# Kernel tuning notes

Measured on AMD Instinct MI355X. Metric: run time of the kernel, lower is better.

## Reference

```python
import jax, jax.numpy as jnp
import numpy as np

BETA = 0.25
SCALE_NUM = 4  # len(latents_scale)


def setup_inputs() -> dict:
    key = jax.random.key(0)
    kz, ke = jax.random.split(key)
    z = jax.random.normal(kz, (8, 256, 32, 32), dtype=jnp.float32)
    emb_weight = jax.random.normal(ke, (16384, 256), dtype=jnp.float32) * 0.02
    return {"z": z, "emb_weight": emb_weight}


def reference(z, emb_weight):
    # z: [B, C, H, W] with C == vq_embed_dim and H == W (source reshapes with W twice)
    B, C, H, W = z.shape
    z_det = jax.lax.stop_gradient(z)

    # NOTE: in the source, `residual` is flattened ONCE before the scale loop and
    # never updated inside it, so every scale picks the same indices. We compute
    # the nearest-codebook assignment once (identical math, argmin of cdist is
    # invariant under sqrt, so squared distances suffice).
    residual = jnp.transpose(z_det, (0, 2, 3, 1)).reshape(-1, C)  # [N, D], N=B*H*W
    d2 = (jnp.sum(residual * residual, axis=1, keepdims=True)
          - 2.0 * residual @ emb_weight.T
          + jnp.sum(emb_weight * emb_weight, axis=1))  # [N, n_e]
    idx = jnp.argmin(d2, axis=1).reshape(B, W, W)  # [B, W, W]

    quantized = jnp.transpose(emb_weight[idx], (0, 3, 1, 2))  # [B, C, H, W]

    z_hat = jnp.zeros_like(z_det)
    loss = jnp.float32(0.0)
    for _ in range(SCALE_NUM):
        z_hat = z_hat + quantized
        loss = loss + BETA * jnp.mean((jax.lax.stop_gradient(z_hat) - z) ** 2) \
                    + jnp.mean((z_hat - z_det) ** 2)
    loss = loss / SCALE_NUM

    total_idx = jnp.concatenate([idx] * SCALE_NUM, axis=1)  # [B, SCALE_NUM*W, W]
    z_hat_out = z + jax.lax.stop_gradient(z_hat - z)  # straight-through
    return z_hat_out, loss, total_idx
```

## Files before the change

### kernel.cpp

```cpp
#include <hip/hip_runtime.h>

#define D      256
#define N_E    16384
#define NPTS   8192
#define ZOUT   2097152
#define MARGIN 2.0e-2f
#define STRIPS 4

typedef short bf16x8 __attribute__((ext_vector_type(8)));
typedef unsigned short us8 __attribute__((ext_vector_type(8)));
typedef float f32x16 __attribute__((ext_vector_type(16)));
typedef unsigned long long u64;

__device__ __forceinline__ unsigned short f2bf(float x) {
    unsigned int u = __float_as_uint(x);
    return (unsigned short)((u + 0x7FFFu + ((u >> 16) & 1u)) >> 16);
}
__device__ __forceinline__ void gl_lds16(const void* g, void* l) {
    __builtin_amdgcn_global_load_lds(
        (const __attribute__((address_space(1))) unsigned int*)g,
        (__attribute__((address_space(3))) unsigned int*)l, 16, 0, 0);
}

__global__ __launch_bounds__(256) void prep(
    const float* __restrict__ z, const float* __restrict__ emb,
    unsigned short* __restrict__ Zpk, float* __restrict__ Zf32,
    unsigned short* __restrict__ Epk, float* __restrict__ e2) {
    const int t = threadIdx.x;
    if (blockIdx.x < 256) {
        const int n0 = blockIdx.x * 32;
        const int p = t & 31, ks8 = t >> 5;
        const int n = n0 + p;
        const int b = n >> 10, hw = n & 1023;
        const float* zb = z + (size_t)b * 262144 + hw;
        const int k0 = ks8 * 32;
        float v[32];
        #pragma unroll
        for (int kk = 0; kk < 32; ++kk)
            v[kk] = zb[(size_t)(k0 + kk) * 1024];
        #pragma unroll
        for (int i = 0; i < 8; ++i) {
            float4 f = {v[i * 4], v[i * 4 + 1], v[i * 4 + 2], v[i * 4 + 3]};
            *(float4*)(Zf32 + (size_t)n * D + k0 + i * 4) = f;
        }
        const int g = n >> 5;
        #pragma unroll
        for (int i = 0; i < 4; ++i) {
            us8 hv;
            #pragma unroll
            for (int c = 0; c < 8; ++c) hv[c] = f2bf(-2.0f * v[i * 8 + c]);
            const int kabs = k0 + i * 8;
            const int ks = kabs >> 4;
            const int l = (n & 31) + ((kabs >> 3) & 1) * 32;
            *(us8*)(Zpk + ((size_t)(g * 16 + ks) * 64 + l) * 8) = hv;
        }
    } else {
        const int j0 = (blockIdx.x - 256) * 32;
        const int jj = j0 + (t >> 3), q = t & 7;
        const float* row = emb + (size_t)jj * D + q * 32;
        float v[32];
        float s = 0.f;
        #pragma unroll
        for (int i = 0; i < 8; ++i) {
            const float4 x = *(const float4*)(row + i * 4);
            v[i * 4] = x.x; v[i * 4 + 1] = x.y; v[i * 4 + 2] = x.z; v[i * 4 + 3] = x.w;
            s += x.x * x.x + x.y * x.y + x.z * x.z + x.w * x.w;
        }
        const int g = jj >> 5;
        #pragma unroll
        for (int i = 0; i < 4; ++i) {
            us8 hv;
            #pragma unroll
            for (int c = 0; c < 8; ++c) hv[c] = f2bf(v[i * 8 + c]);
            const int kabs = q * 32 + i * 8;
            const int ks = kabs >> 4;
            const int l = (jj & 31) + ((kabs >> 3) & 1) * 32;
            *(us8*)(Epk + ((size_t)(g * 16 + ks) * 64 + l) * 8) = hv;
        }
        s += __shfl_xor(s, 1);
        s += __shfl_xor(s, 2);
        s += __shfl_xor(s, 4);
        if (q == 0) e2[jj] = s;
    }
}

__global__ __launch_bounds__(256, 2) void mfma_gemm(
    const unsigned short* __restrict__ Epk, const unsigned short* __restrict__ Zpk,
    const float* __restrict__ e2, float* __restrict__ tminv,
    u64* __restrict__ tmask) {
    __shared__ unsigned short Zbuf[64 * 512];

    const int tid = threadIdx.x, lane = tid & 63, wid = tid >> 6;
    const int c32 = lane & 31, l5 = lane >> 5;
    const int n0 = blockIdx.x * 128;
    const int cs0 = blockIdx.y * (STRIPS * 256);

    #pragma unroll
    for (int ks = 0; ks < 16; ++ks)
        gl_lds16(Zpk + ((size_t)((n0 >> 5) + wid) * 16 + ks) * 512 + lane * 8,
                 Zbuf + (wid * 16 + ks) * 512);
    __syncthreads();

    for (int s = 0; s < STRIPS; ++s) {
        const int cb = cs0 + s * 256 + wid * 64;
        const unsigned short* eb = Epk + ((size_t)(cb >> 5) * 16) * 512 + lane * 8;
        const unsigned short* zb = Zbuf + lane * 8;

        f32x16 acc[2][4];
        const f32x16 z16 = {0.f};
        #pragma unroll
        for (int i = 0; i < 2; ++i)
            #pragma unroll
            for (int j = 0; j < 4; ++j) acc[i][j] = z16;

        bf16x8 ec[2], pc[4];
        ec[0] = *(const bf16x8*)(eb);
        ec[1] = *(const bf16x8*)(eb + 16 * 512);
        #pragma unroll
        for (int j = 0; j < 4; ++j) pc[j] = *(const bf16x8*)(zb + (j * 16) * 512);

        #pragma unroll 4
        for (int ks = 0; ks < 16; ++ks) {
            bf16x8 en[2], pn[4];
            if (ks < 15) {
                en[0] = *(const bf16x8*)(eb + (ks + 1) * 512);
                en[1] = *(const bf16x8*)(eb + (16 + ks + 1) * 512);
                #pragma unroll
                for (int j = 0; j < 4; ++j)
                    pn[j] = *(const bf16x8*)(zb + (j * 16 + ks + 1) * 512);
            }
            #pragma unroll
            for (int i = 0; i < 2; ++i)
                #pragma unroll
                for (int j = 0; j < 4; ++j)
                    acc[i][j] = __builtin_amdgcn_mfma_f32_32x32x16_bf16(
                        ec[i], pc[j], acc[i][j], 0, 0, 0);
            if (ks < 15) {
                ec[0] = en[0]; ec[1] = en[1];
                #pragma unroll
                for (int j = 0; j < 4; ++j) pc[j] = pn[j];
            }
        }

        float e2r[2][16];
        #pragma unroll
        for (int i = 0; i < 2; ++i)
            #pragma unroll
            for (int r = 0; r < 16; ++r)
                e2r[i][r] = e2[cb + i * 32 + (r & 3) + 8 * (r >> 2) + 4 * l5];
        #pragma unroll
        for (int j = 0; j < 4; ++j) {
            float m = e2r[0][0] + acc[0][j][0];
            #pragma unroll
            for (int r = 1; r < 16; ++r) m = fminf(m, e2r[0][r] + acc[0][j][r]);
            #pragma unroll
            for (int r = 0; r < 16; ++r) m = fminf(m, e2r[1][r] + acc[1][j][r]);
            m = fminf(m, __shfl_xor(m, 32));
            const float th = m + MARGIN;
            unsigned mk[2];
            #pragma unroll
            for (int i = 0; i < 2; ++i) {
                unsigned mm = 0;
                #pragma unroll
                for (int r = 0; r < 16; ++r) {
                    const int row = (r & 3) + 8 * (r >> 2) + 4 * l5;
                    mm |= (e2r[i][r] + acc[i][j][r] <= th) ? (1u << row) : 0u;
                }
                mk[i] = mm | (unsigned)__shfl_xor((int)mm, 32);
            }
            if (l5 == 0) {
                const size_t pt = (size_t)(n0 + j * 32 + c32);
                tminv[pt * 256 + (cb >> 6)] = m;
                tmask[pt * 256 + (cb >> 6)] = ((u64)mk[1] << 32) | (u64)mk[0];
            }
        }
    }
}

__global__ __launch_bounds__(256) void rescore(
    const float* __restrict__ tminv, const u64* __restrict__ tmask,
    const float* __restrict__ Zf32, const float* __restrict__ emb,
    const float* __restrict__ e2, int* __restrict__ idxf,
    float* __restrict__ out_idx, float* __restrict__ loss) {
    const int tid = threadIdx.x, lane = tid & 63, w = tid >> 6;
    const int n = blockIdx.x * 4 + w;
    if (blockIdx.x == 0 && tid == 0) loss[0] = 0.f;

    const float4 zr = *(const float4*)(Zf32 + (size_t)n * D + lane * 4);
    const float4 tv = *(const float4*)(tminv + (size_t)n * 256 + lane * 4);

    float m1 = fminf(fminf(tv.x, tv.y), fminf(tv.z, tv.w));
    #pragma unroll
    for (int st = 1; st < 64; st <<= 1) m1 = fminf(m1, __shfl_xor(m1, st));
    const float thresh = m1 + MARGIN;

    u64 best = ~0ull;
    const float tva[4] = {tv.x, tv.y, tv.z, tv.w};
    #pragma unroll
    for (int k = 0; k < 4; ++k) {
        u64 gm = __ballot(tva[k] <= thresh);
        while (gm) {
            const int bit = (int)__builtin_ctzll(gm);
            gm &= gm - 1;
            const int g = bit * 4 + k;
            u64 cm = tmask[(size_t)n * 256 + g];
            while (cm) {
                const int r = (int)__builtin_ctzll(cm);
                cm &= cm - 1;
                const int c = g * 64 + r;
                const float4 ev = *(const float4*)(emb + (size_t)c * D + lane * 4);
                float s = zr.x * ev.x + zr.y * ev.y + zr.z * ev.z + zr.w * ev.w;
                #pragma unroll
                for (int st = 1; st < 64; st <<= 1) s += __shfl_xor(s, st);
                const float d = e2[c] - 2.0f * s;
                unsigned int u = __float_as_uint(d);
                u = (u & 0x80000000u) ? ~u : (u | 0x80000000u);
                const u64 key = ((u64)u << 32) | (unsigned int)c;
                if (key < best) best = key;
            }
        }
    }
    if (lane == 0) {
        const int bi = (int)(unsigned int)(best & 0xFFFFFFFFull);
        idxf[n] = bi;
        const int b = n >> 10, hw = n & 1023;
        const float fv = (float)bi;
        #pragma unroll
        for (int sc = 0; sc < 4; ++sc) out_idx[b * 4096 + sc * 1024 + hw] = fv;
    }
}

__global__ __launch_bounds__(256) void quant_loss(
    const float* __restrict__ z, const float* __restrict__ emb,
    const int* __restrict__ idxf, float* __restrict__ out,
    float* __restrict__ loss) {
    __shared__ int idx_l[32];
    __shared__ float wsum[4];
    const int blk = blockIdx.x;
    const int c0 = (blk >> 8) * 64;
    const int rem = blk & 255;
    const int b = rem >> 5, hw0 = (rem & 31) * 32;
    const int t = threadIdx.x, hw_l = t & 31, cg = t >> 5;
    if (t < 32) idx_l[t] = idxf[b * 1024 + hw0 + t];
    __syncthreads();
    const int j = idx_l[hw_l];
    const float* er = emb + (size_t)j * D + c0 + cg * 8;
    const float4 q0 = *(const float4*)er;
    const float4 q1 = *(const float4*)(er + 4);
    const float qv[8] = {q0.x, q0.y, q0.z, q0.w, q1.x, q1.y, q1.z, q1.w};
    float e = 0.f;
    #pragma unroll
    for (int cc = 0; cc < 8; ++cc) {
        const int c = c0 + cg * 8 + cc;
        const size_t zi = (size_t)b * 262144 + (size_t)c * 1024 + hw0 + hw_l;
        const float zv = z[zi];
        const float q = qv[cc];
        const float zh = ((q + q) + q) + q;
        out[zi] = zv + (zh - zv);
        e += 30.0f * q * q - 20.0f * q * zv + 4.0f * zv * zv;
    }
    #pragma unroll
    for (int off = 32; off > 0; off >>= 1) e += __shfl_down(e, off);
    if ((t & 63) == 0) wsum[t >> 6] = e;
    __syncthreads();
    if (t == 0) {
        const float s = wsum[0] + wsum[1] + wsum[2] + wsum[3];
        atomicAdd(loss, s * (0.3125f / 2097152.0f));
    }
}

extern "C" void kernel_launch(void* const* d_in, const int* in_sizes, int n_in,
                              void* d_out, int out_size, void* d_ws, size_t ws_size,
                              hipStream_t stream) {
    const float* z = (const float*)d_in[0];
    const float* emb = (const float*)d_in[1];
    float* out = (float*)d_out;

    unsigned short* Zpk = (unsigned short*)d_ws;
    unsigned short* Epk = Zpk + (size_t)NPTS * D;
    float* Zf32 = (float*)(Epk + (size_t)N_E * D);
    float* e2 = Zf32 + (size_t)NPTS * D;
    float* tminv = e2 + N_E;
    u64* tmask = (u64*)(tminv + (size_t)NPTS * 256);
    int* idxf = (int*)(tmask + (size_t)NPTS * 256);

    float* loss = out + ZOUT;
    float* out_idx = out + ZOUT + 1;

    prep<<<768, 256, 0, stream>>>(z, emb, Zpk, Zf32, Epk, e2);
    mfma_gemm<<<dim3(NPTS / 128, N_E / (256 * STRIPS)), 256, 0, stream>>>(
        Epk, Zpk, e2, tminv, tmask);
    rescore<<<NPTS / 4, 256, 0, stream>>>(tminv, tmask, Zf32, emb, e2, idxf,
                                          out_idx, loss);
    quant_loss<<<1024, 256, 0, stream>>>(z, emb, idxf, out, loss);
}
```

Before: 176.1 us.

## Fold codebook norms into MFMA, coarsen candidate masks, 4-codeword rescoring

Codebook squared norms are packed as split hi/lo bf16 pairs and added into the accumulators through an extra MFMA against a ones vector, which removes the per-element e2 loads and adds in the epilogue. The candidate mask is coarsened to 16 bits per 64-codeword group, one bit per 4 rows, so tmask shrinks to u16. Rescoring now evaluates 4 codewords at once per wavefront, 16 lanes each, and reduces the keys across lanes. The operand loads in the GEMM loop are double-buffered two steps ahead. In exchange, the coarser masks pull in more false candidates for rescoring, and the bf16 split of e2 lowers the precision of the screening distances.

```diff
diff --git a/kernel.cpp b/kernel.cpp
--- a/kernel.cpp
+++ b/kernel.cpp
@@ -16,6 +16,9 @@
     unsigned int u = __float_as_uint(x);
     return (unsigned short)((u + 0x7FFFu + ((u >> 16) & 1u)) >> 16);
 }
+__device__ __forceinline__ float bf2f(unsigned short h) {
+    return __uint_as_float((unsigned int)h << 16);
+}
 __device__ __forceinline__ void gl_lds16(const void* g, void* l) {
     __builtin_amdgcn_global_load_lds(
         (const __attribute__((address_space(1))) unsigned int*)g,
@@ -25,7 +28,9 @@
 __global__ __launch_bounds__(256) void prep(
     const float* __restrict__ z, const float* __restrict__ emb,
     unsigned short* __restrict__ Zpk, float* __restrict__ Zf32,
-    unsigned short* __restrict__ Epk, float* __restrict__ e2) {
+    unsigned short* __restrict__ Epk, float* __restrict__ e2,
+    unsigned short* __restrict__ E2pk) {
+    __shared__ float sh[32];
     const int t = threadIdx.x;
     if (blockIdx.x < 256) {
         const int n0 = blockIdx.x * 32;
@@ -80,14 +85,27 @@
         s += __shfl_xor(s, 1);
         s += __shfl_xor(s, 2);
         s += __shfl_xor(s, 4);
-        if (q == 0) e2[jj] = s;
+        if (q == 0) { e2[jj] = s; sh[t >> 3] = s; }
+        __syncthreads();
+        if (t < 64) {
+            us8 hv;
+            #pragma unroll
+            for (int c = 0; c < 8; ++c) hv[c] = 0;
+            if (t < 32) {
+                const float vv = sh[t];
+                const unsigned short hi = f2bf(vv);
+                hv[0] = hi;
+                hv[1] = f2bf(vv - bf2f(hi));
+            }
+            *(us8*)(E2pk + (size_t)(blockIdx.x - 256) * 512 + t * 8) = hv;
+        }
     }
 }
 
 __global__ __launch_bounds__(256, 2) void mfma_gemm(
     const unsigned short* __restrict__ Epk, const unsigned short* __restrict__ Zpk,
-    const float* __restrict__ e2, float* __restrict__ tminv,
-    u64* __restrict__ tmask) {
+    const unsigned short* __restrict__ E2pk, float* __restrict__ tminv,
+    unsigned short* __restrict__ tmask) {
     __shared__ unsigned short Zbuf[64 * 512];
 
     const int tid = threadIdx.x, lane = tid & 63, wid = tid >> 6;
@@ -95,6 +113,12 @@
     const int n0 = blockIdx.x * 128;
     const int cs0 = blockIdx.y * (STRIPS * 256);
 
+    us8 puu;
+    #pragma unroll
+    for (int c = 0; c < 8; ++c) puu[c] = 0;
+    if (l5 == 0) { puu[0] = 0x3F80; puu[1] = 0x3F80; }
+    const bf16x8 pu = (bf16x8)puu;
+
     #pragma unroll
     for (int ks = 0; ks < 16; ++ks)
         gl_lds16(Zpk + ((size_t)((n0 >> 5) + wid) * 16 + ks) * 512 + lane * 8,
@@ -106,6 +130,9 @@
         const unsigned short* eb = Epk + ((size_t)(cb >> 5) * 16) * 512 + lane * 8;
         const unsigned short* zb = Zbuf + lane * 8;
 
+        const bf16x8 e2f0 = *(const bf16x8*)(E2pk + (size_t)(cb >> 5) * 512 + lane * 8);
+        const bf16x8 e2f1 = *(const bf16x8*)(E2pk + ((size_t)(cb >> 5) + 1) * 512 + lane * 8);
+
         f32x16 acc[2][4];
         const f32x16 z16 = {0.f};
         #pragma unroll
@@ -113,72 +140,80 @@
             #pragma unroll
             for (int j = 0; j < 4; ++j) acc[i][j] = z16;
 
-        bf16x8 ec[2], pc[4];
-        ec[0] = *(const bf16x8*)(eb);
-        ec[1] = *(const bf16x8*)(eb + 16 * 512);
-        #pragma unroll
-        for (int j = 0; j < 4; ++j) pc[j] = *(const bf16x8*)(zb + (j * 16) * 512);
+        bf16x8 eq[2][2], pq[2][4];
+        #pragma unroll
+        for (int par = 0; par < 2; ++par) {
+            eq[par][0] = *(const bf16x8*)(eb + par * 512);
+            eq[par][1] = *(const bf16x8*)(eb + (16 + par) * 512);
+            #pragma unroll
+            for (int j = 0; j < 4; ++j)
+                pq[par][j] = *(const bf16x8*)(zb + (j * 16 + par) * 512);
+        }
 
         #pragma unroll 4
         for (int ks = 0; ks < 16; ++ks) {
-            bf16x8 en[2], pn[4];
-            if (ks < 15) {
-                en[0] = *(const bf16x8*)(eb + (ks + 1) * 512);
-                en[1] = *(const bf16x8*)(eb + (16 + ks + 1) * 512);
+            const int p = ks & 1;
+            const bf16x8 ec0 = eq[p][0], ec1 = eq[p][1];
+            const bf16x8 pc0 = pq[p][0], pc1 = pq[p][1];
+            const bf16x8 pc2 = pq[p][2], pc3 = pq[p][3];
+            if (ks < 14) {
+                eq[p][0] = *(const bf16x8*)(eb + (ks + 2) * 512);
+                eq[p][1] = *(const bf16x8*)(eb + (16 + ks + 2) * 512);
                 #pragma unroll
                 for (int j = 0; j < 4; ++j)
-                    pn[j] = *(const bf16x8*)(zb + (j * 16 + ks + 1) * 512);
+                    pq[p][j] = *(const bf16x8*)(zb + (j * 16 + ks + 2) * 512);
             }
+            acc[0][0] = __builtin_amdgcn_mfma_f32_32x32x16_bf16(ec0, pc0, acc[0][0], 0, 0, 0);
+            acc[0][1] = __builtin_amdgcn_mfma_f32_32x32x16_bf16(ec0, pc1, acc[0][1], 0, 0, 0);
+            acc[0][2] = __builtin_amdgcn_mfma_f32_32x32x16_bf16(ec0, pc2, acc[0][2], 0, 0, 0);
+            acc[0][3] = __builtin_amdgcn_mfma_f32_32x32x16_bf16(ec0, pc3, acc[0][3], 0, 0, 0);
+            acc[1][0] = __builtin_amdgcn_mfma_f32_32x32x16_bf16(ec1, pc0, acc[1][0], 0, 0, 0);
+            acc[1][1] = __builtin_amdgcn_mfma_f32_32x32x16_bf16(ec1, pc1, acc[1][1], 0, 0, 0);
+            acc[1][2] = __builtin_amdgcn_mfma_f32_32x32x16_bf16(ec1, pc2, acc[1][2], 0, 0, 0);
+            acc[1][3] = __builtin_amdgcn_mfma_f32_32x32x16_bf16(ec1, pc3, acc[1][3], 0, 0, 0);
+        }
+        #pragma unroll
+        for (int j = 0; j < 4; ++j) {
+            acc[0][j] = __builtin_amdgcn_mfma_f32_32x32x16_bf16(e2f0, pu, acc[0][j], 0, 0, 0);
+            acc[1][j] = __builtin_amdgcn_mfma_f32_32x32x16_bf16(e2f1, pu, acc[1][j], 0, 0, 0);
+        }
+
+        #pragma unroll
+        for (int j = 0; j < 4; ++j) {
+            float cm[2][4];
             #pragma unroll
             for (int i = 0; i < 2; ++i)
                 #pragma unroll
-                for (int j = 0; j < 4; ++j)
-                    acc[i][j] = __builtin_amdgcn_mfma_f32_32x32x16_bf16(
-                        ec[i], pc[j], acc[i][j], 0, 0, 0);
-            if (ks < 15) {
-                ec[0] = en[0]; ec[1] = en[1];
-                #pragma unroll
-                for (int j = 0; j < 4; ++j) pc[j] = pn[j];
-            }
-        }
-
-        float e2r[2][16];
-        #pragma unroll
-        for (int i = 0; i < 2; ++i)
-            #pragma unroll
-            for (int r = 0; r < 16; ++r)
-                e2r[i][r] = e2[cb + i * 32 + (r & 3) + 8 * (r >> 2) + 4 * l5];
-        #pragma unroll
-        for (int j = 0; j < 4; ++j) {
-            float m = e2r[0][0] + acc[0][j][0];
-            #pragma unroll
-            for (int r = 1; r < 16; ++r) m = fminf(m, e2r[0][r] + acc[0][j][r]);
-            #pragma unroll
-            for (int r = 0; r < 16; ++r) m = fminf(m, e2r[1][r] + acc[1][j][r]);
+                for (int q = 0; q < 4; ++q) {
+                    float t0 = fminf(acc[i][j][q * 4], acc[i][j][q * 4 + 1]);
+                    t0 = fminf(t0, acc[i][j][q * 4 + 2]);
+                    cm[i][q] = fminf(t0, acc[i][j][q * 4 + 3]);
+                }
+            float m = fminf(cm[0][0], cm[0][1]);
+            m = fminf(m, cm[0][2]); m = fminf(m, cm[0][3]);
+            m = fminf(m, cm[1][0]); m = fminf(m, cm[1][1]);
+            m = fminf(m, cm[1][2]); m = fminf(m, cm[1][3]);
             m = fminf(m, __shfl_xor(m, 32));
             const float th = m + MARGIN;
-            unsigned mk[2];
-            #pragma unroll
-            for (int i = 0; i < 2; ++i) {
-                unsigned mm = 0;
+            unsigned mm = 0;
+            #pragma unroll
+            for (int i = 0; i < 2; ++i)
                 #pragma unroll
-                for (int r = 0; r < 16; ++r) {
-                    const int row = (r & 3) + 8 * (r >> 2) + 4 * l5;
-                    mm |= (e2r[i][r] + acc[i][j][r] <= th) ? (1u << row) : 0u;
-                }
-                mk[i] = mm | (unsigned)__shfl_xor((int)mm, 32);
-            }
+                for (int q = 0; q < 4; ++q)
+                    mm |= (cm[i][q] <= th) ? (1u << (i * 8 + 2 * q)) : 0u;
+            mm <<= l5;
+            mm |= (unsigned)__shfl_xor((int)mm, 32);
             if (l5 == 0) {
                 const size_t pt = (size_t)(n0 + j * 32 + c32);
                 tminv[pt * 256 + (cb >> 6)] = m;
-                tmask[pt * 256 + (cb >> 6)] = ((u64)mk[1] << 32) | (u64)mk[0];
+                tmask[pt * 256 + (cb >> 6)] = (unsigned short)mm;
             }
         }
     }
 }
 
 __global__ __launch_bounds__(256) void rescore(
-    const float* __restrict__ tminv, const u64* __restrict__ tmask,
+    const float* __restrict__ tminv, const unsigned short* __restrict__ tmask,
     const float* __restrict__ Zf32, const float* __restrict__ emb,
     const float* __restrict__ e2, int* __restrict__ idxf,
     float* __restrict__ out_idx, float* __restrict__ loss) {
@@ -186,9 +221,13 @@
     const int n = blockIdx.x * 4 + w;
     if (blockIdx.x == 0 && tid == 0) loss[0] = 0.f;
 
-    const float4 zr = *(const float4*)(Zf32 + (size_t)n * D + lane * 4);
+    const int sl = lane & 15, qr = lane >> 4;
+    float4 zs[4];
+    #pragma unroll
+    for (int p = 0; p < 4; ++p)
+        zs[p] = *(const float4*)(Zf32 + (size_t)n * D + p * 64 + sl * 4);
+
     const float4 tv = *(const float4*)(tminv + (size_t)n * 256 + lane * 4);
-
     float m1 = fminf(fminf(tv.x, tv.y), fminf(tv.z, tv.w));
     #pragma unroll
     for (int st = 1; st < 64; st <<= 1) m1 = fminf(m1, __shfl_xor(m1, st));
@@ -203,19 +242,30 @@
             const int bit = (int)__builtin_ctzll(gm);
             gm &= gm - 1;
             const int g = bit * 4 + k;
-            u64 cm = tmask[(size_t)n * 256 + g];
+            unsigned cm = tmask[(size_t)n * 256 + g];
             while (cm) {
-                const int r = (int)__builtin_ctzll(cm);
+                const int cl = (int)__builtin_ctz(cm);
                 cm &= cm - 1;
-                const int c = g * 64 + r;
-                const float4 ev = *(const float4*)(emb + (size_t)c * D + lane * 4);
-                float s = zr.x * ev.x + zr.y * ev.y + zr.z * ev.z + zr.w * ev.w;
+                const int c0 = g * 64 + cl * 4;
+                const int c = c0 + qr;
+                const float* er = emb + (size_t)c * D;
+                float sacc = 0.f;
                 #pragma unroll
-                for (int st = 1; st < 64; st <<= 1) s += __shfl_xor(s, st);
-                const float d = e2[c] - 2.0f * s;
+                for (int p = 0; p < 4; ++p) {
+                    const float4 ev = *(const float4*)(er + p * 64 + sl * 4);
+                    sacc += ev.x * zs[p].x + ev.y * zs[p].y +
+                            ev.z * zs[p].z + ev.w * zs[p].w;
+                }
+                sacc += __shfl_xor(sacc, 1);
+                sacc += __shfl_xor(sacc, 2);
+                sacc += __shfl_xor(sacc, 4);
+                sacc += __shfl_xor(sacc, 8);
+                const float d = e2[c] - 2.0f * sacc;
                 unsigned int u = __float_as_uint(d);
                 u = (u & 0x80000000u) ? ~u : (u | 0x80000000u);
-                const u64 key = ((u64)u << 32) | (unsigned int)c;
+                u64 key = ((u64)u << 32) | (unsigned int)c;
+                u64 o = __shfl_xor(key, 16); if (o < key) key = o;
+                o = __shfl_xor(key, 32); if (o < key) key = o;
                 if (key < best) best = key;
             }
         }
@@ -281,15 +331,16 @@
     float* Zf32 = (float*)(Epk + (size_t)N_E * D);
     float* e2 = Zf32 + (size_t)NPTS * D;
     float* tminv = e2 + N_E;
-    u64* tmask = (u64*)(tminv + (size_t)NPTS * 256);
-    int* idxf = (int*)(tmask + (size_t)NPTS * 256);
+    unsigned short* tmask = (unsigned short*)(tminv + (size_t)NPTS * 256);
+    unsigned short* E2pk = tmask + (size_t)NPTS * 256;
+    int* idxf = (int*)(E2pk + (size_t)512 * 512);
 
     float* loss = out + ZOUT;
     float* out_idx = out + ZOUT + 1;
 
-    prep<<<768, 256, 0, stream>>>(z, emb, Zpk, Zf32, Epk, e2);
+    prep<<<768, 256, 0, stream>>>(z, emb, Zpk, Zf32, Epk, e2, E2pk);
     mfma_gemm<<<dim3(NPTS / 128, N_E / (256 * STRIPS)), 256, 0, stream>>>(
-        Epk, Zpk, e2, tminv, tmask);
+        Epk, Zpk, E2pk, tminv, tmask);
     rescore<<<NPTS / 4, 256, 0, stream>>>(tminv, tmask, Zf32, emb, e2, idxf,
                                           out_idx, loss);
     quant_loss<<<1024, 256, 0, stream>>>(z, emb, idxf, out, loss);
```

Result: slower. 192.1 us (+9.1%).

## Fuse rescore and quantize-loss kernels into one per-32-point block kernel

Applied to the files above, without the earlier changes.

Merges the candidate rescoring kernel and the quantization/loss kernel into a single kernel with 1024-thread blocks covering 32 points. The selected indices stay in shared memory instead of going through a global index buffer, which removes one launch and one global round trip. Loss zeroing moves into the prep kernel. The grid shrinks to 256 large blocks, each wave handling two points serially, which may lower parallelism and occupancy for the irregular rescoring loop.

```diff
diff --git a/kernel.cpp b/kernel.cpp
--- a/kernel.cpp
+++ b/kernel.cpp
@@ -25,8 +25,10 @@
 __global__ __launch_bounds__(256) void prep(
     const float* __restrict__ z, const float* __restrict__ emb,
     unsigned short* __restrict__ Zpk, float* __restrict__ Zf32,
-    unsigned short* __restrict__ Epk, float* __restrict__ e2) {
+    unsigned short* __restrict__ Epk, float* __restrict__ e2,
+    float* __restrict__ loss) {
     const int t = threadIdx.x;
+    if (blockIdx.x == 0 && t == 0) loss[0] = 0.f;
     if (blockIdx.x < 256) {
         const int n0 = blockIdx.x * 32;
         const int p = t & 31, ks8 = t >> 5;
@@ -177,81 +179,77 @@
     }
 }
 
-__global__ __launch_bounds__(256) void rescore(
+__global__ __launch_bounds__(1024) void rescore_quant(
     const float* __restrict__ tminv, const u64* __restrict__ tmask,
     const float* __restrict__ Zf32, const float* __restrict__ emb,
-    const float* __restrict__ e2, int* __restrict__ idxf,
-    float* __restrict__ out_idx, float* __restrict__ loss) {
-    const int tid = threadIdx.x, lane = tid & 63, w = tid >> 6;
-    const int n = blockIdx.x * 4 + w;
-    if (blockIdx.x == 0 && tid == 0) loss[0] = 0.f;
-
-    const float4 zr = *(const float4*)(Zf32 + (size_t)n * D + lane * 4);
-    const float4 tv = *(const float4*)(tminv + (size_t)n * 256 + lane * 4);
-
-    float m1 = fminf(fminf(tv.x, tv.y), fminf(tv.z, tv.w));
-    #pragma unroll
-    for (int st = 1; st < 64; st <<= 1) m1 = fminf(m1, __shfl_xor(m1, st));
-    const float thresh = m1 + MARGIN;
-
-    u64 best = ~0ull;
-    const float tva[4] = {tv.x, tv.y, tv.z, tv.w};
-    #pragma unroll
-    for (int k = 0; k < 4; ++k) {
-        u64 gm = __ballot(tva[k] <= thresh);
-        while (gm) {
-            const int bit = (int)__builtin_ctzll(gm);
-            gm &= gm - 1;
-            const int g = bit * 4 + k;
-            u64 cm = tmask[(size_t)n * 256 + g];
-            while (cm) {
-                const int r = (int)__builtin_ctzll(cm);
-                cm &= cm - 1;
-                const int c = g * 64 + r;
-                const float4 ev = *(const float4*)(emb + (size_t)c * D + lane * 4);
-                float s = zr.x * ev.x + zr.y * ev.y + zr.z * ev.z + zr.w * ev.w;
-                #pragma unroll
-                for (int st = 1; st < 64; st <<= 1) s += __shfl_xor(s, st);
-                const float d = e2[c] - 2.0f * s;
-                unsigned int u = __float_as_uint(d);
-                u = (u & 0x80000000u) ? ~u : (u | 0x80000000u);
-                const u64 key = ((u64)u << 32) | (unsigned int)c;
-                if (key < best) best = key;
-            }
-        }
-    }
-    if (lane == 0) {
-        const int bi = (int)(unsigned int)(best & 0xFFFFFFFFull);
-        idxf[n] = bi;
-        const int b = n >> 10, hw = n & 1023;
-        const float fv = (float)bi;
-        #pragma unroll
-        for (int sc = 0; sc < 4; ++sc) out_idx[b * 4096 + sc * 1024 + hw] = fv;
-    }
-}
-
-__global__ __launch_bounds__(256) void quant_loss(
-    const float* __restrict__ z, const float* __restrict__ emb,
-    const int* __restrict__ idxf, float* __restrict__ out,
+    const float* __restrict__ e2, const float* __restrict__ z,
+    float* __restrict__ out, float* __restrict__ out_idx,
     float* __restrict__ loss) {
-    __shared__ int idx_l[32];
-    __shared__ float wsum[4];
-    const int blk = blockIdx.x;
-    const int c0 = (blk >> 8) * 64;
-    const int rem = blk & 255;
-    const int b = rem >> 5, hw0 = (rem & 31) * 32;
-    const int t = threadIdx.x, hw_l = t & 31, cg = t >> 5;
-    if (t < 32) idx_l[t] = idxf[b * 1024 + hw0 + t];
+    __shared__ int idx_s[32];
+    __shared__ float wsum[16];
+    const int tid = threadIdx.x, lane = tid & 63, wd = tid >> 6;
+    const int n0 = blockIdx.x * 32;
+    const int b = n0 >> 10, hw0 = n0 & 1023;
+
+    #pragma unroll 1
+    for (int p = 0; p < 2; ++p) {
+        const int lp = wd * 2 + p;
+        const int n = n0 + lp;
+        const float4 zr = *(const float4*)(Zf32 + (size_t)n * D + lane * 4);
+        const float4 tv = *(const float4*)(tminv + (size_t)n * 256 + lane * 4);
+
+        float m1 = fminf(fminf(tv.x, tv.y), fminf(tv.z, tv.w));
+        #pragma unroll
+        for (int st = 1; st < 64; st <<= 1) m1 = fminf(m1, __shfl_xor(m1, st));
+        const float thresh = m1 + MARGIN;
+
+        u64 best = ~0ull;
+        const float tva[4] = {tv.x, tv.y, tv.z, tv.w};
+        #pragma unroll
+        for (int k = 0; k < 4; ++k) {
+            u64 gm = __ballot(tva[k] <= thresh);
+            while (gm) {
+                const int bit = (int)__builtin_ctzll(gm);
+                gm &= gm - 1;
+                const int g = bit * 4 + k;
+                u64 cm = tmask[(size_t)n * 256 + g];
+                while (cm) {
+                    const int r = (int)__builtin_ctzll(cm);
+                    cm &= cm - 1;
+                    const int c = g * 64 + r;
+                    const float4 ev = *(const float4*)(emb + (size_t)c * D + lane * 4);
+                    float s = zr.x * ev.x + zr.y * ev.y + zr.z * ev.z + zr.w * ev.w;
+                    #pragma unroll
+                    for (int st = 1; st < 64; st <<= 1) s += __shfl_xor(s, st);
+                    const float d = e2[c] - 2.0f * s;
+                    unsigned int u = __float_as_uint(d);
+                    u = (u & 0x80000000u) ? ~u : (u | 0x80000000u);
+                    const u64 key = ((u64)u << 32) | (unsigned int)c;
+                    if (key < best) best = key;
+                }
+            }
+        }
+        if (lane == 0)
+            idx_s[lp] = (int)(unsigned int)(best & 0xFFFFFFFFull);
+    }
     __syncthreads();
-    const int j = idx_l[hw_l];
-    const float* er = emb + (size_t)j * D + c0 + cg * 8;
+
+    if (tid < 32) {
+        const float fv = (float)idx_s[tid];
+        #pragma unroll
+        for (int sc = 0; sc < 4; ++sc)
+            out_idx[b * 4096 + sc * 1024 + hw0 + tid] = fv;
+    }
+    const int hw_l = tid & 31, cg = tid >> 5;
+    const int j = idx_s[hw_l];
+    const float* er = emb + (size_t)j * D + cg * 8;
     const float4 q0 = *(const float4*)er;
     const float4 q1 = *(const float4*)(er + 4);
     const float qv[8] = {q0.x, q0.y, q0.z, q0.w, q1.x, q1.y, q1.z, q1.w};
     float e = 0.f;
     #pragma unroll
     for (int cc = 0; cc < 8; ++cc) {
-        const int c = c0 + cg * 8 + cc;
+        const int c = cg * 8 + cc;
         const size_t zi = (size_t)b * 262144 + (size_t)c * 1024 + hw0 + hw_l;
         const float zv = z[zi];
         const float q = qv[cc];
@@ -261,10 +259,12 @@
     }
     #pragma unroll
     for (int off = 32; off > 0; off >>= 1) e += __shfl_down(e, off);
-    if ((t & 63) == 0) wsum[t >> 6] = e;
+    if (lane == 0) wsum[wd] = e;
     __syncthreads();
-    if (t == 0) {
-        const float s = wsum[0] + wsum[1] + wsum[2] + wsum[3];
+    if (tid == 0) {
+        float s = 0.f;
+        #pragma unroll
+        for (int i = 0; i < 16; ++i) s += wsum[i];
         atomicAdd(loss, s * (0.3125f / 2097152.0f));
     }
 }
@@ -282,15 +282,13 @@
     float* e2 = Zf32 + (size_t)NPTS * D;
     float* tminv = e2 + N_E;
     u64* tmask = (u64*)(tminv + (size_t)NPTS * 256);
-    int* idxf = (int*)(tmask + (size_t)NPTS * 256);
 
     float* loss = out + ZOUT;
     float* out_idx = out + ZOUT + 1;
 
-    prep<<<768, 256, 0, stream>>>(z, emb, Zpk, Zf32, Epk, e2);
+    prep<<<768, 256, 0, stream>>>(z, emb, Zpk, Zf32, Epk, e2, loss);
     mfma_gemm<<<dim3(NPTS / 128, N_E / (256 * STRIPS)), 256, 0, stream>>>(
         Epk, Zpk, e2, tminv, tmask);
-    rescore<<<NPTS / 4, 256, 0, stream>>>(tminv, tmask, Zf32, emb, e2, idxf,
-                                          out_idx, loss);
-    quant_loss<<<1024, 256, 0, stream>>>(z, emb, idxf, out, loss);
-}
+    rescore_quant<<<256, 1024, 0, stream>>>(tminv, tmask, Zf32, emb, e2, z,
+                                            out, out_idx, loss);
+}
```

Result: faster. 161.9 us (-8.1%).
